# Optimization experiments

Hardware: AMD Instinct MI355X
Metric: run time of the kernel (lower is better)

The kernel has to match this reference:

```python
import jax, jax.numpy as jnp
import numpy as np

D = 256
NL = 2048
NP = 16384
B = 32
NEG = -1e9


def _layernorm(x, g, b, eps=1e-5):
    mu = x.mean(-1, keepdims=True)
    var = ((x - mu) ** 2).mean(-1, keepdims=True)
    return (x - mu) / jnp.sqrt(var + eps) * g + b


def _cdist(a, b):
    # pairwise euclidean distances, [Na, Nb]
    d2 = (a * a).sum(-1)[:, None] + (b * b).sum(-1)[None, :] - 2.0 * (a @ b.T)
    return jnp.sqrt(jnp.maximum(d2, 1e-12))


def setup_inputs() -> dict:
    key = jax.random.key(0)
    ks = jax.random.split(key, 24)
    init = lambda k, shape: jax.random.normal(k, shape, jnp.float32) / np.float32(np.sqrt(shape[-1]))
    inp = {
        "lig": jax.random.normal(ks[0], (NL, D), jnp.float32),
        "pro": jax.random.normal(ks[1], (NP, D), jnp.float32),
        "lig_pos": jax.random.normal(ks[2], (NL, 3), jnp.float32),
        "pro_pos": jax.random.normal(ks[3], (NP, 3), jnp.float32),
        "lig_batch": jnp.sort(jax.random.randint(ks[4], (NL,), 0, B, jnp.int32)),
        "pro_batch": jnp.sort(jax.random.randint(ks[5], (NP,), 0, B, jnp.int32)),
        "Wq_lig": init(ks[6], (D, D)),
        "Wk_pro": init(ks[7], (D, D)),
        "Wv_pro": init(ks[8], (D, D)),
        "Wq_pro": init(ks[9], (D, D)),
        "Wk_lig": init(ks[10], (D, D)),
        "Wv_lig": init(ks[11], (D, D)),
        "Wout_lig": init(ks[12], (D, D)),
        "bout_lig": jnp.zeros((D,), jnp.float32),
        "Wout_pro": init(ks[13], (D, D)),
        "bout_pro": jnp.zeros((D,), jnp.float32),
        "g_lig": jnp.ones((D,), jnp.float32),
        "b_lig": jnp.zeros((D,), jnp.float32),
        "g_pro": jnp.ones((D,), jnp.float32),
        "b_pro": jnp.zeros((D,), jnp.float32),
    }
    return inp


def reference(lig, pro, lig_pos, pro_pos, lig_batch, pro_batch,
              Wq_lig, Wk_pro, Wv_pro, Wq_pro, Wk_lig, Wv_lig,
              Wout_lig, bout_lig, Wout_pro, bout_pro,
              g_lig, b_lig, g_pro, b_pro):
    scale = jnp.float32(np.sqrt(D))
    # block-diagonal structure via batch-id mask; each row has >=1 valid col
    mask = lig_batch[:, None] == pro_batch[None, :]  # [NL, NP]
    dist_bias = jnp.exp(-_cdist(lig_pos, pro_pos) / 10.0)  # [NL, NP]

    # ligand <- protein
    Q = lig @ Wq_lig.T
    K = pro @ Wk_pro.T
    V = pro @ Wv_pro.T
    scores = Q @ K.T / scale + dist_bias
    attn = jax.nn.softmax(jnp.where(mask, scores, NEG), axis=-1)
    l_ctx = attn @ V
    lig_out = _layernorm(lig + l_ctx @ Wout_lig.T + bout_lig, g_lig, b_lig)

    # protein <- ligand
    Q2 = pro @ Wq_pro.T
    K2 = lig @ Wk_lig.T
    V2 = lig @ Wv_lig.T
    scores2 = Q2 @ K2.T / scale + dist_bias.T
    attn2 = jax.nn.softmax(jnp.where(mask.T, scores2, NEG), axis=-1)
    p_ctx = attn2 @ V2
    pro_out = _layernorm(pro + p_ctx @ Wout_pro.T + bout_pro, g_pro, b_pro)

    return lig_out, pro_out
```

## Files before the change

kernel.cpp:

```cpp
#include <hip/hip_runtime.h>

static constexpr int NLr = 2048;
static constexpr int NPr = 16384;
static constexpr int DIM = 256;
static constexpr int NB  = 32;

typedef unsigned short bf16_t;
using bf16x8 = __attribute__((ext_vector_type(8))) short;
using f32x4  = __attribute__((ext_vector_type(4))) float;

__device__ inline float bf2f(bf16_t u){
  union { unsigned int i; float f; } c; c.i = ((unsigned int)u) << 16; return c.f;
}
__device__ inline bf16_t f2bf(float f){
  union { float f; unsigned int i; } c; c.f = f;
  unsigned int x = c.i;
  return (bf16_t)((x + 0x7fffu + ((x >> 16) & 1u)) >> 16);
}
__device__ inline float wave_sum(float x){
  #pragma unroll
  for (int off = 32; off; off >>= 1) x += __shfl_xor(x, off, 64);
  return x;
}
__device__ inline bf16x8 ldfrag_f32(const float* p){
  float4 a = *reinterpret_cast<const float4*>(p);
  float4 b = *reinterpret_cast<const float4*>(p + 4);
  bf16x8 r;
  r[0]=(short)f2bf(a.x); r[1]=(short)f2bf(a.y); r[2]=(short)f2bf(a.z); r[3]=(short)f2bf(a.w);
  r[4]=(short)f2bf(b.x); r[5]=(short)f2bf(b.y); r[6]=(short)f2bf(b.z); r[7]=(short)f2bf(b.w);
  return r;
}
__device__ inline void hilo8(const float* p, bf16x8& hi, bf16x8& lo){
  #pragma unroll
  for (int i = 0; i < 8; i++){
    float v = p[i];
    bf16_t h = f2bf(v);
    hi[i] = (short)h;
    lo[i] = (short)f2bf(v - bf2f(h));
  }
}

static constexpr int OPART_OFF = 524288;

__global__ void bounds_kernel(const int* __restrict__ lb, const int* __restrict__ pb,
                              int* __restrict__ ls, int* __restrict__ ps){
  int t = threadIdx.x;
  if (t <= NB){
    int lo = 0, hi = NLr;
    while (lo < hi){ int mid = (lo + hi) >> 1; if (lb[mid] < t) lo = mid + 1; else hi = mid; }
    ls[t] = lo;
    lo = 0; hi = NPr;
    while (lo < hi){ int mid = (lo + hi) >> 1; if (pb[mid] < t) lo = mid + 1; else hi = mid; }
    ps[t] = lo;
  }
}

__global__ __launch_bounds__(256) void wprod4(
    const float* __restrict__ Wq_lig, const float* __restrict__ Wk_pro,
    const float* __restrict__ Wk_lig, const float* __restrict__ Wq_pro,
    const float* __restrict__ Wout_lig, const float* __restrict__ Wv_pro,
    const float* __restrict__ Wout_pro, const float* __restrict__ Wv_lig,
    bf16_t* __restrict__ A1, bf16_t* __restrict__ B2,
    bf16_t* __restrict__ PtTL, bf16_t* __restrict__ PtTP){
  __shared__ float Sa[1088];
  __shared__ float Sb[1088];
  const int z = blockIdx.z;
  const float *A, *B; bf16_t* C;
  if      (z == 0){ A = Wq_lig;   B = Wk_pro; C = A1;   }
  else if (z == 1){ A = Wk_lig;   B = Wq_pro; C = B2;   }
  else if (z == 2){ A = Wout_lig; B = Wv_pro; C = PtTL; }
  else            { A = Wout_pro; B = Wv_lig; C = PtTP; }
  const int t  = threadIdx.x;
  const int tx = t & 15, ty = t >> 4;
  const int bm = blockIdx.x, bn = blockIdx.y;
  float acc[4][4] = {};
  if (z < 2){
    float (*As)[68] = (float(*)[68])Sa;
    float (*Bs)[68] = (float(*)[68])Sb;
    const int kk = t >> 4, c0 = (t & 15) << 2;
    for (int kt = 0; kt < DIM; kt += 16){
      float4 av = *reinterpret_cast<const float4*>(A + (size_t)(kt+kk)*DIM + bm*64 + c0);
      float4 bv = *reinterpret_cast<const float4*>(B + (size_t)(kt+kk)*DIM + bn*64 + c0);
      As[kk][c0+0]=av.x; As[kk][c0+1]=av.y; As[kk][c0+2]=av.z; As[kk][c0+3]=av.w;
      Bs[kk][c0+0]=bv.x; Bs[kk][c0+1]=bv.y; Bs[kk][c0+2]=bv.z; Bs[kk][c0+3]=bv.w;
      __syncthreads();
      #pragma unroll
      for (int k = 0; k < 16; k++){
        float a[4], b[4];
        #pragma unroll
        for (int i = 0; i < 4; i++) a[i] = As[k][ty*4+i];
        #pragma unroll
        for (int j = 0; j < 4; j++) b[j] = Bs[k][tx*4+j];
        #pragma unroll
        for (int i = 0; i < 4; i++)
          #pragma unroll
          for (int j = 0; j < 4; j++) acc[i][j] += a[i]*b[j];
      }
      __syncthreads();
    }
  } else {
    float (*As)[17] = (float(*)[17])Sa;
    float (*Bs)[68] = (float(*)[68])Sb;
    const int r  = t >> 2, k0 = (t & 3) << 2;
    const int kk = t >> 4, c0 = (t & 15) << 2;
    for (int kt = 0; kt < DIM; kt += 16){
      float4 av = *reinterpret_cast<const float4*>(A + (size_t)(bm*64+r)*DIM + kt + k0);
      float4 bv = *reinterpret_cast<const float4*>(B + (size_t)(kt+kk)*DIM + bn*64 + c0);
      As[r][k0+0]=av.x; As[r][k0+1]=av.y; As[r][k0+2]=av.z; As[r][k0+3]=av.w;
      Bs[kk][c0+0]=bv.x; Bs[kk][c0+1]=bv.y; Bs[kk][c0+2]=bv.z; Bs[kk][c0+3]=bv.w;
      __syncthreads();
      #pragma unroll
      for (int k = 0; k < 16; k++){
        float a[4], b[4];
        #pragma unroll
        for (int i = 0; i < 4; i++) a[i] = As[ty*4+i][k];
        #pragma unroll
        for (int j = 0; j < 4; j++) b[j] = Bs[k][tx*4+j];
        #pragma unroll
        for (int i = 0; i < 4; i++)
          #pragma unroll
          for (int j = 0; j < 4; j++) acc[i][j] += a[i]*b[j];
      }
      __syncthreads();
    }
  }
  #pragma unroll
  for (int i = 0; i < 4; i++){
    ushort4 o;
    o.x=f2bf(acc[i][0]); o.y=f2bf(acc[i][1]); o.z=f2bf(acc[i][2]); o.w=f2bf(acc[i][3]);
    *reinterpret_cast<ushort4*>(C + (size_t)(bm*64+ty*4+i)*DIM + bn*64 + tx*4) = o;
  }
}

__global__ __launch_bounds__(256) void gemm2(
    const float* __restrict__ A, const bf16_t* __restrict__ Ba, const bf16_t* __restrict__ Bb,
    bf16_t* __restrict__ Ca, bf16_t* __restrict__ Cb){
  const bf16_t* B = blockIdx.z ? Bb : Ba;
  bf16_t*       C = blockIdx.z ? Cb : Ca;
  __shared__ float As[64][17];
  __shared__ float Bs[16][68];
  const int t  = threadIdx.x;
  const int r  = t >> 2, k0 = (t & 3) << 2;
  const int kk = t >> 4, c0 = (t & 15) << 2;
  const int tx = t & 15, ty = t >> 4;
  const int bm = blockIdx.x, bn = blockIdx.y;
  float acc[4][4] = {};
  for (int kt = 0; kt < DIM; kt += 16){
    float4 av = *reinterpret_cast<const float4*>(A + (size_t)(bm*64+r)*DIM + kt + k0);
    ushort4 bu = *reinterpret_cast<const ushort4*>(B + (size_t)(kt+kk)*DIM + bn*64 + c0);
    As[r][k0+0]=av.x; As[r][k0+1]=av.y; As[r][k0+2]=av.z; As[r][k0+3]=av.w;
    Bs[kk][c0+0]=bf2f(bu.x); Bs[kk][c0+1]=bf2f(bu.y);
    Bs[kk][c0+2]=bf2f(bu.z); Bs[kk][c0+3]=bf2f(bu.w);
    __syncthreads();
    #pragma unroll
    for (int k = 0; k < 16; k++){
      float a[4], b[4];
      #pragma unroll
      for (int i = 0; i < 4; i++) a[i] = As[ty*4+i][k];
      #pragma unroll
      for (int j = 0; j < 4; j++) b[j] = Bs[k][tx*4+j];
      #pragma unroll
      for (int i = 0; i < 4; i++)
        #pragma unroll
        for (int j = 0; j < 4; j++) acc[i][j] += a[i]*b[j];
    }
    __syncthreads();
  }
  #pragma unroll
  for (int i = 0; i < 4; i++){
    ushort4 o;
    o.x=f2bf(acc[i][0]); o.y=f2bf(acc[i][1]); o.z=f2bf(acc[i][2]); o.w=f2bf(acc[i][3]);
    *reinterpret_cast<ushort4*>(C + (size_t)(bm*64+ty*4+i)*DIM + bn*64 + tx*4) = o;
  }
}

__global__ __launch_bounds__(128) void attn_lig(
    const bf16_t* __restrict__ Qb, const float* __restrict__ Kf,
    const float* __restrict__ posA, const float* __restrict__ posB,
    const int* __restrict__ batchA, const int* __restrict__ startB,
    float* __restrict__ dout, float* __restrict__ mlpart, int NK){
  __shared__ __align__(16) char raw[36864];
  __shared__ bf16_t Pbuf[2][16][40];
  __shared__ float  mlb[2][2][16];
  bf16_t* Vlds = (bf16_t*)raw;
  float*  Ob   = (float*)raw;
  float* Opart = dout + OPART_OFF;

  const int t = threadIdx.x, wl = t >> 6, lane = t & 63;
  const int qrow = lane & 15, q4 = lane >> 4;
  const int pidx = blockIdx.x, tile = pidx >> 3, split = pidx & 7;
  const int row0 = tile * 16;

  const int rb = batchA[row0 + qrow];
  const int j0 = startB[rb], j1 = startB[rb + 1];
  const float ax = posA[(size_t)(row0+qrow)*3+0];
  const float ay = posA[(size_t)(row0+qrow)*3+1];
  const float az = posA[(size_t)(row0+qrow)*3+2];
  const int kmin = startB[batchA[row0]];
  const int kmax = startB[batchA[row0 + 15] + 1];
  const int base = kmin & ~63;

  bf16x8 qf[8];
  #pragma unroll
  for (int s = 0; s < 8; s++)
    qf[s] = *reinterpret_cast<const bf16x8*>(Qb + (size_t)(row0+qrow)*DIM + s*32 + q4*8);

  f32x4 O[16];
  #pragma unroll
  for (int i = 0; i < 16; i++) O[i] = (f32x4){0.f,0.f,0.f,0.f};
  float m_ = -3.0e38f, l_ = 0.f;

  for (int c = base + split*64; c < kmax; c += 512){
    __syncthreads();
    {
      const int key = t & 63, half = t >> 6;
      const float* src = Kf + (size_t)min(c + key, NK-1)*DIM + half*128;
      #pragma unroll
      for (int gch = 0; gch < 4; gch++){
        float4 tmp[8];
        #pragma unroll
        for (int u = 0; u < 8; u++)
          tmp[u] = *reinterpret_cast<const float4*>(src + gch*32 + u*4);
        #pragma unroll
        for (int u = 0; u < 8; u++){
          int d = half*128 + gch*32 + u*4;
          Vlds[(d+0)*72 + key] = f2bf(tmp[u].x);
          Vlds[(d+1)*72 + key] = f2bf(tmp[u].y);
          Vlds[(d+2)*72 + key] = f2bf(tmp[u].z);
          Vlds[(d+3)*72 + key] = f2bf(tmp[u].w);
        }
      }
    }
    __syncthreads();

    const int kc0 = c + wl*32, colbase = wl*32;
    f32x4 a0 = (f32x4){0.f,0.f,0.f,0.f}, a1 = a0;
    const float* kr0 = Kf + (size_t)min(kc0 + qrow,      NK-1)*DIM;
    const float* kr1 = Kf + (size_t)min(kc0 + 16 + qrow, NK-1)*DIM;
    #pragma unroll
    for (int s = 0; s < 8; s++){
      bf16x8 ka = ldfrag_f32(kr0 + s*32 + q4*8);
      bf16x8 kb = ldfrag_f32(kr1 + s*32 + q4*8);
      a0 = __builtin_amdgcn_mfma_f32_16x16x32_bf16(ka, qf[s], a0, 0, 0, 0);
      a1 = __builtin_amdgcn_mfma_f32_16x16x32_bf16(kb, qf[s], a1, 0, 0, 0);
    }
    float sc[2][4]; bool vm[2][4];
    float cm = -3.0e38f;
    #pragma unroll
    for (int h = 0; h < 2; h++)
      #pragma unroll
      for (int r = 0; r < 4; r++){
        int key = kc0 + h*16 + q4*4 + r;
        bool vld = (key >= j0) && (key < j1);
        int kc = min(key, NK-1);
        float bx = posB[(size_t)kc*3+0], by = posB[(size_t)kc*3+1], bz = posB[(size_t)kc*3+2];
        float dx = ax-bx, dy = ay-by, dz = az-bz;
        float dist = sqrtf(fmaxf(dx*dx + dy*dy + dz*dz, 1e-12f));
        float sv = (h ? a1[r] : a0[r]) * 0.0625f + __expf(-0.1f*dist);
        sc[h][r] = vld ? sv : -3.0e38f;
        vm[h][r] = vld;
        cm = fmaxf(cm, sc[h][r]);
      }
    cm = fmaxf(cm, __shfl_xor(cm, 16));
    cm = fmaxf(cm, __shfl_xor(cm, 32));
    float mn = fmaxf(m_, cm);
    float aa = __expf(m_ - mn);
    float p[2][4]; float ps = 0.f;
    #pragma unroll
    for (int h = 0; h < 2; h++)
      #pragma unroll
      for (int r = 0; r < 4; r++){
        p[h][r] = vm[h][r] ? __expf(sc[h][r] - mn) : 0.f;
        ps += p[h][r];
      }
    ps += __shfl_xor(ps, 16);
    ps += __shfl_xor(ps, 32);
    l_ = l_*aa + ps;
    m_ = mn;
    ushort4 w0, w1;
    w0.x=f2bf(p[0][0]); w0.y=f2bf(p[0][1]); w0.z=f2bf(p[0][2]); w0.w=f2bf(p[0][3]);
    w1.x=f2bf(p[1][0]); w1.y=f2bf(p[1][1]); w1.z=f2bf(p[1][2]); w1.w=f2bf(p[1][3]);
    *reinterpret_cast<ushort4*>(&Pbuf[wl][qrow][q4*4])      = w0;
    *reinterpret_cast<ushort4*>(&Pbuf[wl][qrow][16 + q4*4]) = w1;
    float af0 = __shfl(aa, q4*4+0), af1 = __shfl(aa, q4*4+1);
    float af2 = __shfl(aa, q4*4+2), af3 = __shfl(aa, q4*4+3);
    #pragma unroll
    for (int i = 0; i < 16; i++){
      O[i][0]*=af0; O[i][1]*=af1; O[i][2]*=af2; O[i][3]*=af3;
    }
    bf16x8 pa = *reinterpret_cast<const bf16x8*>(&Pbuf[wl][qrow][q4*8]);
    #pragma unroll
    for (int i = 0; i < 16; i++){
      const bf16_t* vp = Vlds + (size_t)(i*16 + qrow)*72 + colbase + q4*8;
      bf16x8 vb = *reinterpret_cast<const bf16x8*>(vp);
      O[i] = __builtin_amdgcn_mfma_f32_16x16x32_bf16(pa, vb, O[i], 0, 0, 0);
    }
  }

  __syncthreads();
  if (lane < 16){ mlb[wl][0][lane] = m_; mlb[wl][1][lane] = l_; }
  #pragma unroll
  for (int i = 0; i < 16; i++)
    #pragma unroll
    for (int r = 0; r < 4; r++)
      Ob[wl*4096 + (q4*4+r)*256 + i*16 + qrow] = O[i][r];
  __syncthreads();
  for (int e = t; e < 4096; e += 128){
    int row = e >> 8, d = e & 255;
    float m0 = mlb[0][0][row], m1 = mlb[1][0][row];
    float mg = fmaxf(m0, m1);
    float f0 = __expf(m0 - mg), f1 = __expf(m1 - mg);
    Opart[(size_t)pidx*4096 + row*256 + d] = Ob[row*256 + d]*f0 + Ob[4096 + row*256 + d]*f1;
  }
  if (t < 16){
    float m0 = mlb[0][0][t], l0 = mlb[0][1][t];
    float m1 = mlb[1][0][t], l1 = mlb[1][1][t];
    float mg = fmaxf(m0, m1);
    mlpart[pidx*32 + t]      = mg;
    mlpart[pidx*32 + 16 + t] = l0*__expf(m0-mg) + l1*__expf(m1-mg);
  }
}

__global__ __launch_bounds__(128) void merge_lig(
    const float* __restrict__ dpart, const float* __restrict__ mlpart,
    const bf16_t* __restrict__ PtT,
    const float* __restrict__ X, const float* __restrict__ bo,
    const float* __restrict__ g, const float* __restrict__ bb,
    float* __restrict__ out){
  __shared__ float ctxl[16*260];
  __shared__ float Yb[16*260];
  __shared__ float wgt[8][16];
  __shared__ float dens[16];
  const float* Opart = dpart + OPART_OFF;
  const int t = threadIdx.x, wl = t >> 6, lane = t & 63;
  const int qrow = lane & 15, q4 = lane >> 4;
  const int tile = blockIdx.x, row0 = tile*16;
  if (t < 16){
    float mm[8], ll[8], mg = -3.0e38f;
    #pragma unroll
    for (int s = 0; s < 8; s++){
      mm[s] = mlpart[(tile*8+s)*32 + t];
      ll[s] = mlpart[(tile*8+s)*32 + 16 + t];
      mg = fmaxf(mg, mm[s]);
    }
    float den = 0.f;
    #pragma unroll
    for (int s = 0; s < 8; s++){
      float w = __expf(mm[s] - mg);
      wgt[s][t] = w;
      den += ll[s]*w;
    }
    dens[t] = den;
  }
  __syncthreads();
  for (int e = t; e < 4096; e += 128){
    int row = e >> 8, d = e & 255;
    float acc = 0.f;
    #pragma unroll
    for (int s = 0; s < 8; s++)
      acc += Opart[((size_t)(tile*8+s))*4096 + row*256 + d] * wgt[s][row];
    float dd = dens[row];
    ctxl[row*260 + d] = (dd > 0.f) ? acc/dd : 0.f;
  }
  __syncthreads();
  f32x4 Y[8];
  #pragma unroll
  for (int i = 0; i < 8; i++) Y[i] = (f32x4){0.f,0.f,0.f,0.f};
  #pragma unroll
  for (int s = 0; s < 8; s++){
    bf16x8 ca, cl;
    hilo8(ctxl + qrow*260 + s*32 + q4*8, ca, cl);
    #pragma unroll
    for (int tt = 0; tt < 8; tt++){
      const bf16_t* pb = PtT + (size_t)((wl*8+tt)*16 + qrow)*DIM + s*32 + q4*8;
      bf16x8 mb = *reinterpret_cast<const bf16x8*>(pb);
      Y[tt] = __builtin_amdgcn_mfma_f32_16x16x32_bf16(ca, mb, Y[tt], 0, 0, 0);
      Y[tt] = __builtin_amdgcn_mfma_f32_16x16x32_bf16(cl, mb, Y[tt], 0, 0, 0);
    }
  }
  #pragma unroll
  for (int tt = 0; tt < 8; tt++)
    #pragma unroll
    for (int r = 0; r < 4; r++)
      Yb[(q4*4+r)*260 + (wl*8+tt)*16 + qrow] = Y[tt][r];
  __syncthreads();
  for (int i = 0; i < 8; i++){
    int r = wl*8 + i, grow = row0 + r;
    float4 yv = *reinterpret_cast<const float4*>(&Yb[r*260 + 4*lane]);
    float4 xv = *reinterpret_cast<const float4*>(X  + (size_t)grow*DIM + 4*lane);
    float4 bv = *reinterpret_cast<const float4*>(bo + 4*lane);
    float4 gv = *reinterpret_cast<const float4*>(g  + 4*lane);
    float4 b2 = *reinterpret_cast<const float4*>(bb + 4*lane);
    float v0 = xv.x + yv.x + bv.x, v1 = xv.y + yv.y + bv.y;
    float v2 = xv.z + yv.z + bv.z, v3 = xv.w + yv.w + bv.w;
    float sum = wave_sum(v0+v1+v2+v3);
    float ssq = wave_sum(v0*v0+v1*v1+v2*v2+v3*v3);
    float mu  = sum * (1.0f/DIM);
    float var = ssq * (1.0f/DIM) - mu*mu;
    float rr  = rsqrtf(fmaxf(var, 0.f) + 1e-5f);
    float4 o;
    o.x = (v0-mu)*rr*gv.x + b2.x;
    o.y = (v1-mu)*rr*gv.y + b2.y;
    o.z = (v2-mu)*rr*gv.z + b2.z;
    o.w = (v3-mu)*rr*gv.w + b2.w;
    *reinterpret_cast<float4*>(out + (size_t)grow*DIM + 4*lane) = o;
  }
}

__global__ __launch_bounds__(128) void attn_pro(
    const float* __restrict__ Qf, const bf16_t* __restrict__ Kb,
    const float* __restrict__ Vf,
    const float* __restrict__ posA, const float* __restrict__ posB,
    const int* __restrict__ batchA, const int* __restrict__ startB,
    const bf16_t* __restrict__ PtT,
    const float* __restrict__ X, const float* __restrict__ bo,
    const float* __restrict__ g, const float* __restrict__ bb,
    float* __restrict__ out, int out_off, int NK){
  __shared__ __align__(16) char raw[33280];
  __shared__ bf16_t Pbuf[2][16][40];
  bf16_t* Vlds = (bf16_t*)raw;
  float*  ctxl = (float*)raw;

  const int t = threadIdx.x, wl = t >> 6, lane = t & 63;
  const int qrow = lane & 15, q4 = lane >> 4;
  const int row0b = blockIdx.x * 32, row0 = row0b + wl*16;

  const int rb = batchA[row0 + qrow];
  const int j0 = startB[rb], j1 = startB[rb + 1];
  const float ax = posA[(size_t)(row0+qrow)*3+0];
  const float ay = posA[(size_t)(row0+qrow)*3+1];
  const float az = posA[(size_t)(row0+qrow)*3+2];
  const int kmin = startB[batchA[row0b]];
  const int kmax = startB[batchA[row0b + 31] + 1];
  const int base = kmin & ~31;

  bf16x8 qf[8], ql[8];
  #pragma unroll
  for (int s = 0; s < 8; s++)
    hilo8(Qf + (size_t)(row0+qrow)*DIM + s*32 + q4*8, qf[s], ql[s]);

  f32x4 O[16];
  #pragma unroll
  for (int i = 0; i < 16; i++) O[i] = (f32x4){0.f,0.f,0.f,0.f};
  float m_ = -3.0e38f, l_ = 0.f;

  for (int c = base; c < kmax; c += 32){
    __syncthreads();
    {
      const int key = t & 31, qtr = t >> 5;
      const float* src = Vf + (size_t)min(c + key, NK-1)*DIM + qtr*64;
      #pragma unroll
      for (int gch = 0; gch < 2; gch++){
        float4 tmp[8];
        #pragma unroll
        for (int u = 0; u < 8; u++)
          tmp[u] = *reinterpret_cast<const float4*>(src + gch*32 + u*4);
        #pragma unroll
        for (int u = 0; u < 8; u++){
          int d = qtr*64 + gch*32 + u*4;
          Vlds[(d+0)*40 + key] = f2bf(tmp[u].x);
          Vlds[(d+1)*40 + key] = f2bf(tmp[u].y);
          Vlds[(d+2)*40 + key] = f2bf(tmp[u].z);
          Vlds[(d+3)*40 + key] = f2bf(tmp[u].w);
        }
      }
    }
    __syncthreads();

    f32x4 a0 = (f32x4){0.f,0.f,0.f,0.f}, a1 = a0;
    const bf16_t* kr0 = Kb + (size_t)min(c + qrow,      NK-1)*DIM;
    const bf16_t* kr1 = Kb + (size_t)min(c + 16 + qrow, NK-1)*DIM;
    #pragma unroll
    for (int s = 0; s < 8; s++){
      bf16x8 ka = *reinterpret_cast<const bf16x8*>(kr0 + s*32 + q4*8);
      bf16x8 kb = *reinterpret_cast<const bf16x8*>(kr1 + s*32 + q4*8);
      a0 = __builtin_amdgcn_mfma_f32_16x16x32_bf16(ka, qf[s], a0, 0, 0, 0);
      a1 = __builtin_amdgcn_mfma_f32_16x16x32_bf16(kb, qf[s], a1, 0, 0, 0);
      a0 = __builtin_amdgcn_mfma_f32_16x16x32_bf16(ka, ql[s], a0, 0, 0, 0);
      a1 = __builtin_amdgcn_mfma_f32_16x16x32_bf16(kb, ql[s], a1, 0, 0, 0);
    }
    float sc[2][4]; bool vm[2][4];
    float cm = -3.0e38f;
    #pragma unroll
    for (int h = 0; h < 2; h++)
      #pragma unroll
      for (int r = 0; r < 4; r++){
        int key = c + h*16 + q4*4 + r;
        bool vld = (key >= j0) && (key < j1);
        int kc = min(key, NK-1);
        float bx = posB[(size_t)kc*3+0], by = posB[(size_t)kc*3+1], bz = posB[(size_t)kc*3+2];
        float dx = ax-bx, dy = ay-by, dz = az-bz;
        float dist = sqrtf(fmaxf(dx*dx + dy*dy + dz*dz, 1e-12f));
        float sv = (h ? a1[r] : a0[r]) * 0.0625f + __expf(-0.1f*dist);
        sc[h][r] = vld ? sv : -3.0e38f;
        vm[h][r] = vld;
        cm = fmaxf(cm, sc[h][r]);
      }
    cm = fmaxf(cm, __shfl_xor(cm, 16));
    cm = fmaxf(cm, __shfl_xor(cm, 32));
    float mn = fmaxf(m_, cm);
    float aa = __expf(m_ - mn);
    float p[2][4]; float ps = 0.f;
    #pragma unroll
    for (int h = 0; h < 2; h++)
      #pragma unroll
      for (int r = 0; r < 4; r++){
        p[h][r] = vm[h][r] ? __expf(sc[h][r] - mn) : 0.f;
        ps += p[h][r];
      }
    ps += __shfl_xor(ps, 16);
    ps += __shfl_xor(ps, 32);
    l_ = l_*aa + ps;
    m_ = mn;
    ushort4 w0, w1;
    w0.x=f2bf(p[0][0]); w0.y=f2bf(p[0][1]); w0.z=f2bf(p[0][2]); w0.w=f2bf(p[0][3]);
    w1.x=f2bf(p[1][0]); w1.y=f2bf(p[1][1]); w1.z=f2bf(p[1][2]); w1.w=f2bf(p[1][3]);
    *reinterpret_cast<ushort4*>(&Pbuf[wl][qrow][q4*4])      = w0;
    *reinterpret_cast<ushort4*>(&Pbuf[wl][qrow][16 + q4*4]) = w1;
    float af0 = __shfl(aa, q4*4+0), af1 = __shfl(aa, q4*4+1);
    float af2 = __shfl(aa, q4*4+2), af3 = __shfl(aa, q4*4+3);
    #pragma unroll
    for (int i = 0; i < 16; i++){
      O[i][0]*=af0; O[i][1]*=af1; O[i][2]*=af2; O[i][3]*=af3;
    }
    bf16x8 pa = *reinterpret_cast<const bf16x8*>(&Pbuf[wl][qrow][q4*8]);
    #pragma unroll
    for (int i = 0; i < 16; i++){
      const bf16_t* vp = Vlds + (size_t)(i*16 + qrow)*40 + q4*8;
      bf16x8 vb = *reinterpret_cast<const bf16x8*>(vp);
      O[i] = __builtin_amdgcn_mfma_f32_16x16x32_bf16(pa, vb, O[i], 0, 0, 0);
    }
  }

  __syncthreads();
  {
    float lr0 = __shfl(l_, q4*4+0), lr1 = __shfl(l_, q4*4+1);
    float lr2 = __shfl(l_, q4*4+2), lr3 = __shfl(l_, q4*4+3);
    float i0 = lr0>0.f?1.f/lr0:0.f, i1 = lr1>0.f?1.f/lr1:0.f;
    float i2 = lr2>0.f?1.f/lr2:0.f, i3 = lr3>0.f?1.f/lr3:0.f;
    float* cw = ctxl + wl*4160;
    #pragma unroll
    for (int i = 0; i < 16; i++){
      cw[(q4*4+0)*260 + i*16+qrow] = O[i][0]*i0;
      cw[(q4*4+1)*260 + i*16+qrow] = O[i][1]*i1;
      cw[(q4*4+2)*260 + i*16+qrow] = O[i][2]*i2;
      cw[(q4*4+3)*260 + i*16+qrow] = O[i][3]*i3;
    }
  }
  const float* cw = ctxl + wl*4160;
  f32x4 Y[16];
  #pragma unroll
  for (int i = 0; i < 16; i++) Y[i] = (f32x4){0.f,0.f,0.f,0.f};
  #pragma unroll
  for (int s = 0; s < 8; s++){
    bf16x8 ca, cl;
    hilo8(cw + qrow*260 + s*32 + q4*8, ca, cl);
    #pragma unroll
    for (int tt = 0; tt < 16; tt++){
      const bf16_t* pb = PtT + (size_t)(tt*16 + qrow)*DIM + s*32 + q4*8;
      bf16x8 mb = *reinterpret_cast<const bf16x8*>(pb);
      Y[tt] = __builtin_amdgcn_mfma_f32_16x16x32_bf16(ca, mb, Y[tt], 0, 0, 0);
      Y[tt] = __builtin_amdgcn_mfma_f32_16x16x32_bf16(cl, mb, Y[tt], 0, 0, 0);
    }
  }
  float* YB = ctxl + wl*4160;
  #pragma unroll
  for (int tt = 0; tt < 16; tt++)
    #pragma unroll
    for (int r = 0; r < 4; r++)
      YB[(q4*4+r)*260 + tt*16 + qrow] = Y[tt][r];

  for (int i = 0; i < 16; i++){
    int grow = row0 + i;
    float4 yv = *reinterpret_cast<const float4*>(&YB[i*260 + 4*lane]);
    float4 xv = *reinterpret_cast<const float4*>(X  + (size_t)grow*DIM + 4*lane);
    float4 bv = *reinterpret_cast<const float4*>(bo + 4*lane);
    float4 gv = *reinterpret_cast<const float4*>(g  + 4*lane);
    float4 b2 = *reinterpret_cast<const float4*>(bb + 4*lane);
    float v0 = xv.x + yv.x + bv.x, v1 = xv.y + yv.y + bv.y;
    float v2 = xv.z + yv.z + bv.z, v3 = xv.w + yv.w + bv.w;
    float sum = wave_sum(v0+v1+v2+v3);
    float ssq = wave_sum(v0*v0+v1*v1+v2*v2+v3*v3);
    float mu  = sum * (1.0f/DIM);
    float var = ssq * (1.0f/DIM) - mu*mu;
    float rr  = rsqrtf(fmaxf(var, 0.f) + 1e-5f);
    float4 o;
    o.x = (v0-mu)*rr*gv.x + b2.x;
    o.y = (v1-mu)*rr*gv.y + b2.y;
    o.z = (v2-mu)*rr*gv.z + b2.z;
    o.w = (v3-mu)*rr*gv.w + b2.w;
    *reinterpret_cast<float4*>(out + (size_t)out_off + (size_t)grow*DIM + 4*lane) = o;
  }
}

extern "C" void kernel_launch(void* const* d_in, const int* in_sizes, int n_in,
                              void* d_out, int out_size, void* d_ws, size_t ws_size,
                              hipStream_t stream){
  const float* lig      = (const float*)d_in[0];
  const float* pro      = (const float*)d_in[1];
  const float* lig_pos  = (const float*)d_in[2];
  const float* pro_pos  = (const float*)d_in[3];
  const int*   lig_batch= (const int*)d_in[4];
  const int*   pro_batch= (const int*)d_in[5];
  const float* Wq_lig   = (const float*)d_in[6];
  const float* Wk_pro   = (const float*)d_in[7];
  const float* Wv_pro   = (const float*)d_in[8];
  const float* Wq_pro   = (const float*)d_in[9];
  const float* Wk_lig   = (const float*)d_in[10];
  const float* Wv_lig   = (const float*)d_in[11];
  const float* Wout_lig = (const float*)d_in[12];
  const float* bout_lig = (const float*)d_in[13];
  const float* Wout_pro = (const float*)d_in[14];
  const float* bout_pro = (const float*)d_in[15];
  const float* g_lig    = (const float*)d_in[16];
  const float* b_lig    = (const float*)d_in[17];
  const float* g_pro    = (const float*)d_in[18];
  const float* b_pro    = (const float*)d_in[19];

  int* ib        = (int*)d_ws;
  int* lig_start = ib + 16;
  int* pro_start = ib + 56;
  bf16_t* wsb  = ((bf16_t*)d_ws) + 256;
  bf16_t* A1   = wsb;
  bf16_t* B2   = A1   + DIM*DIM;
  bf16_t* PtTL = B2   + DIM*DIM;
  bf16_t* PtTP = PtTL + DIM*DIM;
  bf16_t* G    = PtTP + DIM*DIM;
  bf16_t* T_lig= G    + (size_t)NLr*DIM;
  float* mlpart= (float*)(T_lig + (size_t)NLr*DIM);

  float* outp = (float*)d_out;

  hipLaunchKernelGGL(bounds_kernel, dim3(1), dim3(64), 0, stream,
                     lig_batch, pro_batch, lig_start, pro_start);
  hipLaunchKernelGGL(wprod4, dim3(4,4,4), dim3(256), 0, stream,
                     Wq_lig, Wk_pro, Wk_lig, Wq_pro, Wout_lig, Wv_pro, Wout_pro, Wv_lig,
                     A1, B2, PtTL, PtTP);
  hipLaunchKernelGGL(gemm2, dim3(NLr/64, 4, 2), dim3(256), 0, stream,
                     lig, A1, B2, T_lig, G);

  hipLaunchKernelGGL(attn_lig, dim3(NLr/16*8), dim3(128), 0, stream,
                     T_lig, pro, lig_pos, pro_pos, lig_batch, pro_start, outp, mlpart, NPr);
  hipLaunchKernelGGL(merge_lig, dim3(NLr/16), dim3(128), 0, stream,
                     outp, mlpart, PtTL, lig, bout_lig, g_lig, b_lig, outp);

  hipLaunchKernelGGL(attn_pro, dim3(NPr/32), dim3(128), 0, stream,
                     pro, G, lig, pro_pos, lig_pos, pro_batch, lig_start, PtTP,
                     pro, bout_pro, g_pro, b_pro, outp, NLr*DIM, NLr);
}
```

Measured before the change: 263.0 us.

## Pre-convert protein features to bf16, store partials in bf16, drop bounds kernel

Adds a third z-slice to gemm2 that converts the fp32 protein matrix to bf16 once, stored in scratch space inside the output buffer. attn_lig then reads bf16 K/V directly instead of repeatedly loading fp32 and converting it. Split-KV partial outputs are now written and read as bf16, halving that traffic at some precision cost. The separate bounds kernel is replaced by per-thread binary searches inside the attention kernels, removing one launch but adding redundant searches.

```diff
diff --git a/kernel.cpp b/kernel.cpp
--- a/kernel.cpp
+++ b/kernel.cpp
@@ -21,14 +21,6 @@
   #pragma unroll
   for (int off = 32; off; off >>= 1) x += __shfl_xor(x, off, 64);
   return x;
-}
-__device__ inline bf16x8 ldfrag_f32(const float* p){
-  float4 a = *reinterpret_cast<const float4*>(p);
-  float4 b = *reinterpret_cast<const float4*>(p + 4);
-  bf16x8 r;
-  r[0]=(short)f2bf(a.x); r[1]=(short)f2bf(a.y); r[2]=(short)f2bf(a.z); r[3]=(short)f2bf(a.w);
-  r[4]=(short)f2bf(b.x); r[5]=(short)f2bf(b.y); r[6]=(short)f2bf(b.z); r[7]=(short)f2bf(b.w);
-  return r;
 }
 __device__ inline void hilo8(const float* p, bf16x8& hi, bf16x8& lo){
   #pragma unroll
@@ -39,21 +31,14 @@
     lo[i] = (short)f2bf(v - bf2f(h));
   }
 }
+__device__ inline int lbound(const int* __restrict__ a, int n, int v){
+  int lo = 0, hi = n;
+  while (lo < hi){ int mid = (lo + hi) >> 1; if (a[mid] < v) lo = mid + 1; else hi = mid; }
+  return lo;
+}
 
 static constexpr int OPART_OFF = 524288;
-
-__global__ void bounds_kernel(const int* __restrict__ lb, const int* __restrict__ pb,
-                              int* __restrict__ ls, int* __restrict__ ps){
-  int t = threadIdx.x;
-  if (t <= NB){
-    int lo = 0, hi = NLr;
-    while (lo < hi){ int mid = (lo + hi) >> 1; if (lb[mid] < t) lo = mid + 1; else hi = mid; }
-    ls[t] = lo;
-    lo = 0; hi = NPr;
-    while (lo < hi){ int mid = (lo + hi) >> 1; if (pb[mid] < t) lo = mid + 1; else hi = mid; }
-    ps[t] = lo;
-  }
-}
+static constexpr int PROB_OFF  = 2621440;
 
 __global__ __launch_bounds__(256) void wprod4(
     const float* __restrict__ Wq_lig, const float* __restrict__ Wk_pro,
@@ -134,7 +119,18 @@
 
 __global__ __launch_bounds__(256) void gemm2(
     const float* __restrict__ A, const bf16_t* __restrict__ Ba, const bf16_t* __restrict__ Bb,
-    bf16_t* __restrict__ Ca, bf16_t* __restrict__ Cb){
+    bf16_t* __restrict__ Ca, bf16_t* __restrict__ Cb,
+    const float* __restrict__ pro, bf16_t* __restrict__ proB){
+  if (blockIdx.z == 2){
+    size_t base = ((size_t)(blockIdx.x*4 + blockIdx.y)*256 + threadIdx.x)*4;
+    for (size_t i = base; i < (size_t)NPr*DIM; i += 131072){
+      float4 v = *reinterpret_cast<const float4*>(pro + i);
+      ushort4 o;
+      o.x=f2bf(v.x); o.y=f2bf(v.y); o.z=f2bf(v.z); o.w=f2bf(v.w);
+      *reinterpret_cast<ushort4*>(proB + i) = o;
+    }
+    return;
+  }
   const bf16_t* B = blockIdx.z ? Bb : Ba;
   bf16_t*       C = blockIdx.z ? Cb : Ca;
   __shared__ float As[64][17];
@@ -175,16 +171,16 @@
 }
 
 __global__ __launch_bounds__(128) void attn_lig(
-    const bf16_t* __restrict__ Qb, const float* __restrict__ Kf,
+    const bf16_t* __restrict__ Qb, const bf16_t* __restrict__ Kb,
     const float* __restrict__ posA, const float* __restrict__ posB,
-    const int* __restrict__ batchA, const int* __restrict__ startB,
-    float* __restrict__ dout, float* __restrict__ mlpart, int NK){
+    const int* __restrict__ batchA, const int* __restrict__ pb,
+    float* __restrict__ dout, float* __restrict__ mlpart){
   __shared__ __align__(16) char raw[36864];
   __shared__ bf16_t Pbuf[2][16][40];
   __shared__ float  mlb[2][2][16];
   bf16_t* Vlds = (bf16_t*)raw;
   float*  Ob   = (float*)raw;
-  float* Opart = dout + OPART_OFF;
+  bf16_t* Opart = (bf16_t*)(dout + OPART_OFF);
 
   const int t = threadIdx.x, wl = t >> 6, lane = t & 63;
   const int qrow = lane & 15, q4 = lane >> 4;
@@ -192,12 +188,13 @@
   const int row0 = tile * 16;
 
   const int rb = batchA[row0 + qrow];
-  const int j0 = startB[rb], j1 = startB[rb + 1];
+  const int j0 = lbound(pb, NPr, rb);
+  const int j1 = lbound(pb, NPr, rb + 1);
+  const int kmin = __shfl(j0, 0);
+  const int kmax = __shfl(j1, 15);
   const float ax = posA[(size_t)(row0+qrow)*3+0];
   const float ay = posA[(size_t)(row0+qrow)*3+1];
   const float az = posA[(size_t)(row0+qrow)*3+2];
-  const int kmin = startB[batchA[row0]];
-  const int kmax = startB[batchA[row0 + 15] + 1];
   const int base = kmin & ~63;
 
   bf16x8 qf[8];
@@ -214,20 +211,19 @@
     __syncthreads();
     {
       const int key = t & 63, half = t >> 6;
-      const float* src = Kf + (size_t)min(c + key, NK-1)*DIM + half*128;
-      #pragma unroll
-      for (int gch = 0; gch < 4; gch++){
-        float4 tmp[8];
+      const bf16_t* src = Kb + (size_t)min(c + key, NPr-1)*DIM + half*128;
+      #pragma unroll
+      for (int g = 0; g < 2; g++){
+        bf16x8 tmp[8];
         #pragma unroll
         for (int u = 0; u < 8; u++)
-          tmp[u] = *reinterpret_cast<const float4*>(src + gch*32 + u*4);
+          tmp[u] = *reinterpret_cast<const bf16x8*>(src + g*64 + u*8);
         #pragma unroll
         for (int u = 0; u < 8; u++){
-          int d = half*128 + gch*32 + u*4;
-          Vlds[(d+0)*72 + key] = f2bf(tmp[u].x);
-          Vlds[(d+1)*72 + key] = f2bf(tmp[u].y);
-          Vlds[(d+2)*72 + key] = f2bf(tmp[u].z);
-          Vlds[(d+3)*72 + key] = f2bf(tmp[u].w);
+          int d = half*128 + g*64 + u*8;
+          #pragma unroll
+          for (int jj = 0; jj < 8; jj++)
+            Vlds[(d+jj)*72 + key] = (bf16_t)tmp[u][jj];
         }
       }
     }
@@ -235,12 +231,12 @@
 
     const int kc0 = c + wl*32, colbase = wl*32;
     f32x4 a0 = (f32x4){0.f,0.f,0.f,0.f}, a1 = a0;
-    const float* kr0 = Kf + (size_t)min(kc0 + qrow,      NK-1)*DIM;
-    const float* kr1 = Kf + (size_t)min(kc0 + 16 + qrow, NK-1)*DIM;
+    const bf16_t* kr0 = Kb + (size_t)min(kc0 + qrow,      NPr-1)*DIM;
+    const bf16_t* kr1 = Kb + (size_t)min(kc0 + 16 + qrow, NPr-1)*DIM;
     #pragma unroll
     for (int s = 0; s < 8; s++){
-      bf16x8 ka = ldfrag_f32(kr0 + s*32 + q4*8);
-      bf16x8 kb = ldfrag_f32(kr1 + s*32 + q4*8);
+      bf16x8 ka = *reinterpret_cast<const bf16x8*>(kr0 + s*32 + q4*8);
+      bf16x8 kb = *reinterpret_cast<const bf16x8*>(kr1 + s*32 + q4*8);
       a0 = __builtin_amdgcn_mfma_f32_16x16x32_bf16(ka, qf[s], a0, 0, 0, 0);
       a1 = __builtin_amdgcn_mfma_f32_16x16x32_bf16(kb, qf[s], a1, 0, 0, 0);
     }
@@ -252,7 +248,7 @@
       for (int r = 0; r < 4; r++){
         int key = kc0 + h*16 + q4*4 + r;
         bool vld = (key >= j0) && (key < j1);
-        int kc = min(key, NK-1);
+        int kc = min(key, NPr-1);
         float bx = posB[(size_t)kc*3+0], by = posB[(size_t)kc*3+1], bz = posB[(size_t)kc*3+2];
         float dx = ax-bx, dy = ay-by, dz = az-bz;
         float dist = sqrtf(fmaxf(dx*dx + dy*dy + dz*dz, 1e-12f));
@@ -306,11 +302,11 @@
       Ob[wl*4096 + (q4*4+r)*256 + i*16 + qrow] = O[i][r];
   __syncthreads();
   for (int e = t; e < 4096; e += 128){
-    int row = e >> 8, d = e & 255;
+    int row = e >> 8;
     float m0 = mlb[0][0][row], m1 = mlb[1][0][row];
     float mg = fmaxf(m0, m1);
     float f0 = __expf(m0 - mg), f1 = __expf(m1 - mg);
-    Opart[(size_t)pidx*4096 + row*256 + d] = Ob[row*256 + d]*f0 + Ob[4096 + row*256 + d]*f1;
+    Opart[(size_t)pidx*4096 + e] = f2bf(Ob[e]*f0 + Ob[4096 + e]*f1);
   }
   if (t < 16){
     float m0 = mlb[0][0][t], l0 = mlb[0][1][t];
@@ -331,7 +327,7 @@
   __shared__ float Yb[16*260];
   __shared__ float wgt[8][16];
   __shared__ float dens[16];
-  const float* Opart = dpart + OPART_OFF;
+  const bf16_t* Opart = (const bf16_t*)(dpart + OPART_OFF);
   const int t = threadIdx.x, wl = t >> 6, lane = t & 63;
   const int qrow = lane & 15, q4 = lane >> 4;
   const int tile = blockIdx.x, row0 = tile*16;
@@ -358,7 +354,7 @@
     float acc = 0.f;
     #pragma unroll
     for (int s = 0; s < 8; s++)
-      acc += Opart[((size_t)(tile*8+s))*4096 + row*256 + d] * wgt[s][row];
+      acc += bf2f(Opart[((size_t)(tile*8+s))*4096 + e]) * wgt[s][row];
     float dd = dens[row];
     ctxl[row*260 + d] = (dd > 0.f) ? acc/dd : 0.f;
   }
@@ -411,11 +407,11 @@
     const float* __restrict__ Qf, const bf16_t* __restrict__ Kb,
     const float* __restrict__ Vf,
     const float* __restrict__ posA, const float* __restrict__ posB,
-    const int* __restrict__ batchA, const int* __restrict__ startB,
+    const int* __restrict__ batchA, const int* __restrict__ lb,
     const bf16_t* __restrict__ PtT,
     const float* __restrict__ X, const float* __restrict__ bo,
     const float* __restrict__ g, const float* __restrict__ bb,
-    float* __restrict__ out, int out_off, int NK){
+    float* __restrict__ out, int out_off){
   __shared__ __align__(16) char raw[33280];
   __shared__ bf16_t Pbuf[2][16][40];
   bf16_t* Vlds = (bf16_t*)raw;
@@ -426,12 +422,15 @@
   const int row0b = blockIdx.x * 32, row0 = row0b + wl*16;
 
   const int rb = batchA[row0 + qrow];
-  const int j0 = startB[rb], j1 = startB[rb + 1];
+  const int j0 = lbound(lb, NLr, rb);
+  const int j1 = lbound(lb, NLr, rb + 1);
+  const int bfirst = batchA[row0b];
+  const int blast  = batchA[row0b + 31];
+  const int kmin = lbound(lb, NLr, bfirst);
+  const int kmax = lbound(lb, NLr, blast + 1);
   const float ax = posA[(size_t)(row0+qrow)*3+0];
   const float ay = posA[(size_t)(row0+qrow)*3+1];
   const float az = posA[(size_t)(row0+qrow)*3+2];
-  const int kmin = startB[batchA[row0b]];
-  const int kmax = startB[batchA[row0b + 31] + 1];
   const int base = kmin & ~31;
 
   bf16x8 qf[8], ql[8];
@@ -448,7 +447,7 @@
     __syncthreads();
     {
       const int key = t & 31, qtr = t >> 5;
-      const float* src = Vf + (size_t)min(c + key, NK-1)*DIM + qtr*64;
+      const float* src = Vf + (size_t)min(c + key, NLr-1)*DIM + qtr*64;
       #pragma unroll
       for (int gch = 0; gch < 2; gch++){
         float4 tmp[8];
@@ -468,8 +467,8 @@
     __syncthreads();
 
     f32x4 a0 = (f32x4){0.f,0.f,0.f,0.f}, a1 = a0;
-    const bf16_t* kr0 = Kb + (size_t)min(c + qrow,      NK-1)*DIM;
-    const bf16_t* kr1 = Kb + (size_t)min(c + 16 + qrow, NK-1)*DIM;
+    const bf16_t* kr0 = Kb + (size_t)min(c + qrow,      NLr-1)*DIM;
+    const bf16_t* kr1 = Kb + (size_t)min(c + 16 + qrow, NLr-1)*DIM;
     #pragma unroll
     for (int s = 0; s < 8; s++){
       bf16x8 ka = *reinterpret_cast<const bf16x8*>(kr0 + s*32 + q4*8);
@@ -487,7 +486,7 @@
       for (int r = 0; r < 4; r++){
         int key = c + h*16 + q4*4 + r;
         bool vld = (key >= j0) && (key < j1);
-        int kc = min(key, NK-1);
+        int kc = min(key, NLr-1);
         float bx = posB[(size_t)kc*3+0], by = posB[(size_t)kc*3+1], bz = posB[(size_t)kc*3+2];
         float dx = ax-bx, dy = ay-by, dz = az-bz;
         float dist = sqrtf(fmaxf(dx*dx + dy*dy + dz*dz, 1e-12f));
@@ -617,9 +616,6 @@
   const float* g_pro    = (const float*)d_in[18];
   const float* b_pro    = (const float*)d_in[19];
 
-  int* ib        = (int*)d_ws;
-  int* lig_start = ib + 16;
-  int* pro_start = ib + 56;
   bf16_t* wsb  = ((bf16_t*)d_ws) + 256;
   bf16_t* A1   = wsb;
   bf16_t* B2   = A1   + DIM*DIM;
@@ -630,21 +626,20 @@
   float* mlpart= (float*)(T_lig + (size_t)NLr*DIM);
 
   float* outp = (float*)d_out;
-
-  hipLaunchKernelGGL(bounds_kernel, dim3(1), dim3(64), 0, stream,
-                     lig_batch, pro_batch, lig_start, pro_start);
+  bf16_t* proB = (bf16_t*)(outp + PROB_OFF);
+
   hipLaunchKernelGGL(wprod4, dim3(4,4,4), dim3(256), 0, stream,
                      Wq_lig, Wk_pro, Wk_lig, Wq_pro, Wout_lig, Wv_pro, Wout_pro, Wv_lig,
                      A1, B2, PtTL, PtTP);
-  hipLaunchKernelGGL(gemm2, dim3(NLr/64, 4, 2), dim3(256), 0, stream,
-                     lig, A1, B2, T_lig, G);
+  hipLaunchKernelGGL(gemm2, dim3(NLr/64, 4, 3), dim3(256), 0, stream,
+                     lig, A1, B2, T_lig, G, pro, proB);
 
   hipLaunchKernelGGL(attn_lig, dim3(NLr/16*8), dim3(128), 0, stream,
-                     T_lig, pro, lig_pos, pro_pos, lig_batch, pro_start, outp, mlpart, NPr);
+                     T_lig, proB, lig_pos, pro_pos, lig_batch, pro_batch, outp, mlpart);
   hipLaunchKernelGGL(merge_lig, dim3(NLr/16), dim3(128), 0, stream,
                      outp, mlpart, PtTL, lig, bout_lig, g_lig, b_lig, outp);
 
   hipLaunchKernelGGL(attn_pro, dim3(NPr/32), dim3(128), 0, stream,
-                     pro, G, lig, pro_pos, lig_pos, pro_batch, lig_start, PtTP,
-                     pro, bout_pro, g_pro, b_pro, outp, NLr*DIM, NLr);
-}
+                     pro, G, lig, pro_pos, lig_pos, pro_batch, lig_batch, PtTP,
+                     pro, bout_pro, g_pro, b_pro, outp, NLr*DIM);
+}
```

Result: faster. 247.0 us (-6.1%).
